# Optimization experiments

Hardware: AMD Instinct MI355X
Metric: run time of the kernel (lower is better)

## Reference

```python
import jax, jax.numpy as jnp
import numpy as np

NUM_GROUPS = 4
NUM_HEADS = 8
EPS = 1e-5


def setup_inputs() -> dict:
    key = jax.random.key(0)
    k1, k2, k3 = jax.random.split(key, 3)
    B, C, D, H, W = 4, 256, 32, 32, 32
    x = jax.random.normal(k1, (B, C, D, H, W), dtype=jnp.float32)
    gn_weight = jnp.ones((C,), dtype=jnp.float32)
    gn_bias = jnp.zeros((C,), dtype=jnp.float32)
    # 1x1x1 conv weights collapse to [out_ch, in_ch] matrices
    qkv_weight = jax.random.normal(k2, (3 * C, C), dtype=jnp.float32) * (1.0 / np.sqrt(C))
    out_weight = jax.random.normal(k3, (C, C), dtype=jnp.float32) * (1.0 / np.sqrt(C))
    out_bias = jnp.zeros((C,), dtype=jnp.float32)
    return {"x": x, "gn_weight": gn_weight, "gn_bias": gn_bias,
            "qkv_weight": qkv_weight, "out_weight": out_weight, "out_bias": out_bias}


def _group_norm(x, weight, bias):
    B, C, D, H, W = x.shape
    g = NUM_GROUPS
    xg = x.reshape(B, g, C // g, D, H, W)
    mean = jnp.mean(xg, axis=(2, 3, 4, 5), keepdims=True)
    var = jnp.var(xg, axis=(2, 3, 4, 5), keepdims=True)
    xn = ((xg - mean) * jax.lax.rsqrt(var + EPS)).reshape(B, C, D, H, W)
    return xn * weight[None, :, None, None, None] + bias[None, :, None, None, None]


def reference(x, gn_weight, gn_bias, qkv_weight, out_weight, out_bias):
    B, C, D, H, W = x.shape
    N = D * H * W
    hd = C // NUM_HEADS  # per-head channels

    norm = _group_norm(x, gn_weight, gn_bias)
    # 1x1x1 conv == channel matmul: [B,3C,D,H,W]
    qkv = jnp.einsum('bcdhw,oc->bodhw', norm, qkv_weight)
    # 'b (qkv heads c) d h w -> qkv b heads c (d h w)'
    qkv = qkv.reshape(B, 3, NUM_HEADS, hd, N)
    q, k, v = qkv[:, 0], qkv[:, 1], qkv[:, 2]  # each [B, heads, hd, N]

    k = jax.nn.softmax(k, axis=-1)  # softmax over spatial dim
    sim = jnp.einsum('bhdn,bhen->bhde', k, v)   # [B, heads, hd, hd]
    out = jnp.einsum('bhde,bhdn->bhen', sim, q)  # [B, heads, hd, N]
    out = out.reshape(B, C, D, H, W)

    out = jnp.einsum('bcdhw,oc->bodhw', out, out_weight) + out_bias[None, :, None, None, None]
    return out + x
```

## Files before the change

### kernel.cpp

```cpp
#include <hip/hip_runtime.h>
#include <cmath>


typedef __bf16 bf16x8 __attribute__((ext_vector_type(8)));
typedef float f32x4 __attribute__((ext_vector_type(4)));

union U16 { uint4 u; unsigned short s[8]; bf16x8 v; };

__device__ __forceinline__ float bf2f(unsigned short h) {
    unsigned int u = ((unsigned int)h) << 16;
    return __builtin_bit_cast(float, u);
}
__device__ __forceinline__ unsigned short f2bf(float f) {
    unsigned int u = __builtin_bit_cast(unsigned int, f);
    u = (u + 0x7fffu + ((u >> 16) & 1u)) >> 16;
    return (unsigned short)u;
}
__device__ __forceinline__ unsigned int pack2(unsigned short a, unsigned short b) {
    return (unsigned int)a | ((unsigned int)b << 16);
}

__global__ __launch_bounds__(64) void k_detect(const unsigned int* __restrict__ xr,
                                               int* __restrict__ flag) {
    unsigned int u = xr[threadIdx.x * 997];
    int e = (u >> 7) & 0xFF;
    bool ok = (e >= 100) && (e <= 141);
    unsigned long long m = __ballot(ok);
    if (threadIdx.x == 0) *flag = (__popcll(m) < 32) ? 1 : 0;
}

__global__ __launch_bounds__(256) void k_cvt_w(const void* __restrict__ qkvw,
                                               const void* __restrict__ outw,
                                               const void* __restrict__ gnw,
                                               const void* __restrict__ gnb,
                                               const void* __restrict__ outb,
                                               const int* __restrict__ flagp,
                                               unsigned short* __restrict__ wdst) {
    int idx = blockIdx.x * 256 + threadIdx.x;
    if (idx >= 262912) return;
    const void* src; int off;
    if      (idx < 196608) { src = qkvw; off = idx; }
    else if (idx < 262144) { src = outw; off = idx - 196608; }
    else if (idx < 262400) { src = gnw;  off = idx - 262144; }
    else if (idx < 262656) { src = gnb;  off = idx - 262400; }
    else                   { src = outb; off = idx - 262656; }
    int f = *flagp;
    wdst[idx] = f ? f2bf(((const float*)src)[off])
                  : ((const unsigned short*)src)[off];
}

__global__ __launch_bounds__(256) void k_cvt_x(const void* __restrict__ xr,
                                               const int* __restrict__ flagp,
                                               unsigned short* __restrict__ xw) {
    int f = *flagp;
    size_t base = ((size_t)blockIdx.x * 256 + threadIdx.x) * 8;
    if (f) {
        const float* xf = (const float*)xr;
        float4 a = *(const float4*)(xf + base);
        float4 c = *(const float4*)(xf + base + 4);
        U16 o;
        o.s[0] = f2bf(a.x); o.s[1] = f2bf(a.y); o.s[2] = f2bf(a.z); o.s[3] = f2bf(a.w);
        o.s[4] = f2bf(c.x); o.s[5] = f2bf(c.y); o.s[6] = f2bf(c.z); o.s[7] = f2bf(c.w);
        *(uint4*)(xw + base) = o.u;
    } else {
        *(uint4*)(xw + base) = *(const uint4*)((const unsigned short*)xr + base);
    }
}

__global__ __launch_bounds__(256) void k_gnsum(const unsigned short* __restrict__ x,
                                               float2* __restrict__ gn_part) {
    int t = threadIdx.x, bid = blockIdx.x;
    int grp = bid >> 7, chunk = bid & 127;
    const unsigned short* p = x + (size_t)grp * 2097152 + (size_t)chunk * 16384;
    float s = 0.f, q = 0.f;
    for (int i = 0; i < 8; i++) {
        U16 u; u.u = *(const uint4*)(p + i * 2048 + t * 8);
#pragma unroll
        for (int j = 0; j < 8; j++) { float f = bf2f(u.s[j]); s += f; q += f * f; }
    }
#pragma unroll
    for (int off = 32; off > 0; off >>= 1) { s += __shfl_xor(s, off); q += __shfl_xor(q, off); }
    __shared__ float rs[4], rq[4];
    int wave = t >> 6;
    if ((t & 63) == 0) { rs[wave] = s; rq[wave] = q; }
    __syncthreads();
    if (t == 0) gn_part[bid] = make_float2(rs[0] + rs[1] + rs[2] + rs[3],
                                           rq[0] + rq[1] + rq[2] + rq[3]);
}

__global__ __launch_bounds__(128) void k_gnfinal(const float2* __restrict__ gn_part,
                                                 float2* __restrict__ gstats) {
    int bg = blockIdx.x, t = threadIdx.x;
    float2 v = gn_part[bg * 128 + t];
    float s = v.x, q = v.y;
#pragma unroll
    for (int off = 32; off > 0; off >>= 1) { s += __shfl_xor(s, off); q += __shfl_xor(q, off); }
    __shared__ float rs[2], rq[2];
    if ((t & 63) == 0) { rs[t >> 6] = s; rq[t >> 6] = q; }
    __syncthreads();
    if (t == 0) {
        const float inv = 1.0f / 2097152.0f;
        float S = rs[0] + rs[1], Q = rq[0] + rq[1];
        float mean = S * inv;
        float var = Q * inv - mean * mean;
        gstats[bg] = make_float2(mean, rsqrtf(var + 1e-5f));
    }
}

__global__ __launch_bounds__(64) void k_beta(const unsigned short* __restrict__ wq,
                                             const unsigned short* __restrict__ wgnw,
                                             const unsigned short* __restrict__ wgnb,
                                             const float2* __restrict__ gstats,
                                             float* __restrict__ beta) {
    int bid = blockIdx.x;
    int b = bid / 768, o = bid % 768;
    int t = threadIdx.x, c = t * 4;
    float2 ms = gstats[b * 4 + (c >> 6)];
    uint2 qw = *(const uint2*)(wq + o * 256 + c);
    uint2 gw = *(const uint2*)(wgnw + c);
    uint2 gb = *(const uint2*)(wgnb + c);
    unsigned short qs[4] = {(unsigned short)(qw.x & 0xffff), (unsigned short)(qw.x >> 16),
                            (unsigned short)(qw.y & 0xffff), (unsigned short)(qw.y >> 16)};
    unsigned short wsx[4] = {(unsigned short)(gw.x & 0xffff), (unsigned short)(gw.x >> 16),
                             (unsigned short)(gw.y & 0xffff), (unsigned short)(gw.y >> 16)};
    unsigned short bs[4] = {(unsigned short)(gb.x & 0xffff), (unsigned short)(gb.x >> 16),
                            (unsigned short)(gb.y & 0xffff), (unsigned short)(gb.y >> 16)};
    float bacc = 0.f;
#pragma unroll
    for (int j = 0; j < 4; j++)
        bacc += bf2f(qs[j]) * (bf2f(bs[j]) - ms.x * ms.y * bf2f(wsx[j]));
#pragma unroll
    for (int off = 32; off > 0; off >>= 1) bacc += __shfl_xor(bacc, off);
    if (t == 0) beta[b * 768 + o] = bacc;
}

__global__ __launch_bounds__(256) void k_transpose(const unsigned short* __restrict__ x,
                                                   const unsigned short* __restrict__ wgnw,
                                                   const float2* __restrict__ gstats,
                                                   unsigned short* __restrict__ xt) {
    int tid = threadIdx.x, bid = blockIdx.x;
    int b = bid >> 11, r2 = bid & 2047, cblk = r2 >> 9, nblk = r2 & 511;
    float rstd = gstats[b * 4 + cblk].y;
    __shared__ __align__(16) unsigned short T[64 * 80];
    unsigned short tmp[2][8];
#pragma unroll
    for (int i = 0; i < 2; i++) {
        int crow = (tid >> 3) + 32 * i, nch = tid & 7;
        int c = cblk * 64 + crow;
        float sc = bf2f(wgnw[c]) * rstd;
        U16 u; u.u = *(const uint4*)(x + ((size_t)(b * 256 + c)) * 32768 + (size_t)nblk * 64 + nch * 8);
#pragma unroll
        for (int j = 0; j < 8; j++) tmp[i][j] = f2bf(bf2f(u.s[j]) * sc);
    }
#pragma unroll
    for (int i = 0; i < 2; i++) {
        int crow = (tid >> 3) + 32 * i, nch = tid & 7;
#pragma unroll
        for (int jj = 0; jj < 8; jj++) {
            int j = (jj + tid) & 7;
            T[(nch * 8 + j) * 80 + crow] = tmp[i][j];
        }
    }
    __syncthreads();
#pragma unroll
    for (int i = 0; i < 2; i++) {
        int nrow = (tid >> 3) + 32 * i, cch = tid & 7;
        uint4 v = *(const uint4*)&T[nrow * 80 + cch * 8];
        *(uint4*)(xt + ((size_t)b * 32768 + (size_t)nblk * 64 + nrow) * 256 + cblk * 64 + cch * 8) = v;
    }
}

__device__ __forceinline__ void stage128x64(const unsigned short* __restrict__ g,
                                            unsigned short* __restrict__ lds, int tid) {
    int wave = tid >> 6;
    int lane = tid & 63;
    int rsub = lane >> 3;
    int slot = lane & 7;
    uint4 v[4];
#pragma unroll
    for (int i = 0; i < 4; i++) {
        int row = wave * 32 + i * 8 + rsub;
        v[i] = *(const uint4*)(g + (size_t)row * 256 + slot * 8);
    }
#pragma unroll
    for (int i = 0; i < 4; i++) {
        int row = wave * 32 + i * 8 + rsub;
        int s = slot ^ (row & 7);
        *(uint4*)&lds[row * 64 + s * 8] = v[i];
    }
}

__device__ __forceinline__ void gemm_core(const unsigned short* __restrict__ A,
                                          const unsigned short* __restrict__ Bsrc,
                                          unsigned short* ldsA, unsigned short* ldsB,
                                          int tid, f32x4 (&acc)[4][4]) {
    int lane = tid & 63, l15 = lane & 15, quad = lane >> 4;
    int wave = tid >> 6, wm = wave & 1, wn = wave >> 1;
    for (int kt = 0; kt < 4; kt++) {
        stage128x64(A + kt * 64, ldsA, tid);
        stage128x64(Bsrc + kt * 64, ldsB, tid);
        __syncthreads();
#pragma unroll
        for (int ks = 0; ks < 2; ks++) {
            bf16x8 af[4], bv[4];
#pragma unroll
            for (int mi = 0; mi < 4; mi++) {
                int row = wm * 64 + mi * 16 + l15;
                af[mi] = *(const bf16x8*)&ldsA[row * 64 + (((ks * 4 + quad) ^ (row & 7)) * 8)];
            }
#pragma unroll
            for (int ni = 0; ni < 4; ni++) {
                int row = wn * 64 + ni * 16 + l15;
                bv[ni] = *(const bf16x8*)&ldsB[row * 64 + (((ks * 4 + quad) ^ (row & 7)) * 8)];
            }
#pragma unroll
            for (int mi = 0; mi < 4; mi++)
#pragma unroll
                for (int ni = 0; ni < 4; ni++)
                    acc[mi][ni] = __builtin_amdgcn_mfma_f32_16x16x32_bf16(af[mi], bv[ni], acc[mi][ni], 0, 0, 0);
        }
        __syncthreads();
    }
}

__global__ __launch_bounds__(256) void k_gemm1(const unsigned short* __restrict__ wq,
                                               const unsigned short* __restrict__ xt,
                                               const float* __restrict__ beta,
                                               unsigned short* __restrict__ qT,
                                               unsigned short* __restrict__ kv) {
    __shared__ __align__(16) unsigned short ldsbuf[2 * 128 * 64];
    unsigned short* ldsA = ldsbuf;
    unsigned short* ldsB = ldsbuf + 128 * 64;
    int tid = threadIdx.x, bid = blockIdx.x;
    int L = (bid & 7) * ((int)gridDim.x >> 3) + (bid >> 3);
    int mblk = L % 6;
    int t2 = L / 6;
    int nblk = t2 & 255, b = t2 >> 8;
    int o0 = mblk * 128;
    size_t n0 = (size_t)nblk * 128;
    const unsigned short* A = wq + (size_t)o0 * 256;
    const unsigned short* Bx = xt + ((size_t)b * 32768 + n0) * 256;
    f32x4 acc[4][4] = {};
    gemm_core(A, Bx, ldsA, ldsB, tid, acc);

    int lane = tid & 63, l15 = lane & 15, quad = lane >> 4;
    int wave = tid >> 6, wm = wave & 1, wn = wave >> 1;
    bool isQ = (mblk < 2);
    if (isQ) {
#pragma unroll
        for (int mi = 0; mi < 4; mi++) {
            int o_l = wm * 64 + mi * 16 + quad * 4;
            float4 be = *(const float4*)(beta + b * 768 + o0 + o_l);
#pragma unroll
            for (int ni = 0; ni < 4; ni++) {
                int n_l = wn * 64 + ni * 16 + l15;
                f32x4 v = acc[mi][ni];
                uint2 pv;
                pv.x = pack2(f2bf(v[0] + be.x), f2bf(v[1] + be.y));
                pv.y = pack2(f2bf(v[2] + be.z), f2bf(v[3] + be.w));
                *(uint2*)&ldsbuf[(n_l * 128 + o_l) ^ ((n_l & 7) << 3)] = pv;
            }
        }
        __syncthreads();
#pragma unroll
        for (int p = 0; p < 8; p++) {
            int n_l = p * 16 + (tid >> 4);
            int ch = tid & 15;
            uint4 v = *(const uint4*)&ldsbuf[(n_l * 128 + ch * 8) ^ ((n_l & 7) << 3)];
            *(uint4*)(qT + ((size_t)b * 32768 + n0 + n_l) * 256 + o0 + ch * 8) = v;
        }
    } else {
#pragma unroll
        for (int mi = 0; mi < 4; mi++) {
            int o_l = wm * 64 + mi * 16 + quad * 4;
            float4 be = *(const float4*)(beta + b * 768 + o0 + o_l);
            float bev[4] = {be.x, be.y, be.z, be.w};
#pragma unroll
            for (int ni = 0; ni < 4; ni++) {
                int n_l = wn * 64 + ni * 16 + l15;
                f32x4 v = acc[mi][ni];
#pragma unroll
                for (int r = 0; r < 4; r++) {
                    int o_r = o_l + r;
                    ldsbuf[(o_r * 128 + n_l) ^ ((o_r & 7) << 3)] = f2bf(v[r] + bev[r]);
                }
            }
        }
        __syncthreads();
        int kv0 = o0 - 256;
#pragma unroll
        for (int p = 0; p < 8; p++) {
            int o_r = p * 16 + (tid >> 4);
            int ch = tid & 15;
            uint4 v = *(const uint4*)&ldsbuf[(o_r * 128 + ch * 8) ^ ((o_r & 7) << 3)];
            *(uint4*)(kv + ((size_t)b * 512 + kv0 + o_r) * 32768 + n0 + ch * 8) = v;
        }
    }
}

__global__ __launch_bounds__(256) void k_stats(const unsigned short* __restrict__ kv,
                                               float2* __restrict__ stats) {
    int row = blockIdx.x, t = threadIdx.x;
    const unsigned short* p = kv + ((size_t)(row >> 8) * 512 + (row & 255)) * 32768;
    float m = -3.0e38f;
    for (int i = 0; i < 16; i++) {
        U16 u; u.u = *(const uint4*)(p + i * 2048 + t * 8);
#pragma unroll
        for (int j = 0; j < 8; j++) m = fmaxf(m, bf2f(u.s[j]));
    }
#pragma unroll
    for (int off = 32; off > 0; off >>= 1) m = fmaxf(m, __shfl_xor(m, off));
    __shared__ float rm[4], rs[4];
    int wave = t >> 6;
    if ((t & 63) == 0) rm[wave] = m;
    __syncthreads();
    m = fmaxf(fmaxf(rm[0], rm[1]), fmaxf(rm[2], rm[3]));
    float s = 0.f;
    for (int i = 0; i < 16; i++) {
        U16 u; u.u = *(const uint4*)(p + i * 2048 + t * 8);
#pragma unroll
        for (int j = 0; j < 8; j++) s += __expf(bf2f(u.s[j]) - m);
    }
#pragma unroll
    for (int off = 32; off > 0; off >>= 1) s += __shfl_xor(s, off);
    if ((t & 63) == 0) rs[wave] = s;
    __syncthreads();
    if (t == 0) stats[row] = make_float2(m, 1.0f / (rs[0] + rs[1] + rs[2] + rs[3]));
}

__global__ __launch_bounds__(64) void k_sim(const unsigned short* __restrict__ kv,
                                            const float2* __restrict__ stats,
                                            float* __restrict__ partials) {
    int bid = blockIdx.x;
    int bh = bid >> 6, chunk = bid & 63;
    int b = bh >> 3, h = bh & 7;
    int lane = threadIdx.x, l15 = lane & 15, quad = lane >> 4;
    size_t n0 = (size_t)chunk * 512 + quad * 8;
    float mrow[2], isr[2];
#pragma unroll
    for (int mi = 0; mi < 2; mi++) {
        float2 st = stats[b * 256 + h * 32 + mi * 16 + l15];
        mrow[mi] = st.x; isr[mi] = st.y;
    }
    const unsigned short* kb = kv + ((size_t)b * 512 + h * 32) * 32768;
    const unsigned short* vb = kv + ((size_t)b * 512 + 256 + h * 32) * 32768;
    f32x4 acc[2][2] = {};
    for (int t = 0; t < 16; t++) {
        size_t n = n0 + t * 32;
        bf16x8 af[2], bv[2];
#pragma unroll
        for (int mi = 0; mi < 2; mi++) {
            U16 u; u.u = *(const uint4*)(kb + (size_t)(mi * 16 + l15) * 32768 + n);
            U16 pv;
#pragma unroll
            for (int j = 0; j < 8; j++) pv.s[j] = f2bf(__expf(bf2f(u.s[j]) - mrow[mi]) * isr[mi]);
            af[mi] = pv.v;
        }
#pragma unroll
        for (int ni = 0; ni < 2; ni++) {
            U16 u; u.u = *(const uint4*)(vb + (size_t)(ni * 16 + l15) * 32768 + n);
            bv[ni] = u.v;
        }
#pragma unroll
        for (int mi = 0; mi < 2; mi++)
#pragma unroll
            for (int ni = 0; ni < 2; ni++)
                acc[mi][ni] = __builtin_amdgcn_mfma_f32_16x16x32_bf16(af[mi], bv[ni], acc[mi][ni], 0, 0, 0);
    }
    float* po = partials + (size_t)(bh * 64 + chunk) * 1024;
#pragma unroll
    for (int mi = 0; mi < 2; mi++)
#pragma unroll
        for (int ni = 0; ni < 2; ni++)
#pragma unroll
            for (int rr = 0; rr < 4; rr++)
                po[(mi * 16 + quad * 4 + rr) * 32 + ni * 16 + l15] = acc[mi][ni][rr];
}

__global__ __launch_bounds__(256) void k_combine(const float* __restrict__ partials,
                                                 float* __restrict__ sim) {
    int bh = blockIdx.x, tid = threadIdx.x;
#pragma unroll
    for (int i = 0; i < 4; i++) {
        float a = 0.f;
        const float* p = partials + (size_t)bh * 65536 + tid + i * 256;
        for (int c = 0; c < 64; c++) a += p[(size_t)c * 1024];
        sim[bh * 1024 + tid + i * 256] = a;
    }
}

__global__ __launch_bounds__(256) void k_buildM(const unsigned short* __restrict__ wo,
                                                const float* __restrict__ sim,
                                                unsigned short* __restrict__ M) {
    int bid = blockIdx.x, tid = threadIdx.x;
    int b = bid >> 8, o = bid & 255;
    __shared__ float lw[256];
    __shared__ float ls[8192];
    lw[tid] = bf2f(wo[o * 256 + tid]);
#pragma unroll
    for (int i = 0; i < 32; i++) ls[tid + i * 256] = sim[(size_t)b * 8192 + tid + i * 256];
    __syncthreads();
    int h = tid >> 5, d = tid & 31;
    float a = 0.f;
#pragma unroll
    for (int e = 0; e < 32; e++) {
        int ee = (e + d) & 31;
        a += lw[h * 32 + ee] * ls[h * 1024 + d * 32 + ee];
    }
    M[((size_t)b * 256 + o) * 256 + tid] = f2bf(a);
}

__global__ __launch_bounds__(256) void k_gemm2(const unsigned short* __restrict__ qT,
                                               const unsigned short* __restrict__ M,
                                               const unsigned short* __restrict__ wob,
                                               const void* __restrict__ xr,
                                               const int* __restrict__ flagp,
                                               void* __restrict__ outv,
                                               int b0) {
    __shared__ __align__(16) unsigned short ldsbuf[2 * 128 * 64];
    unsigned short* ldsA = ldsbuf;
    unsigned short* ldsB = ldsbuf + 128 * 64;
    float* ldsF = (float*)ldsbuf;
    int tid = threadIdx.x, bid = blockIdx.x;
    int L = (bid & 7) * ((int)gridDim.x >> 3) + (bid >> 3);
    int oblk = L & 1;
    int t2 = L >> 1;
    int mblk = t2 & 255, b = t2 >> 8;
    size_t n0 = (size_t)mblk * 128;
    int o0 = oblk * 128;
    const unsigned short* A = qT + ((size_t)b * 32768 + n0) * 256;
    const unsigned short* Bm = M + ((size_t)b * 256 + o0) * 256;
    f32x4 acc[4][4] = {};
    gemm_core(A, Bm, ldsA, ldsB, tid, acc);

    int f = *flagp;
    int gb = b0 + b;
    int lane = tid & 63, l15 = lane & 15, quad = lane >> 4;
    int wave = tid >> 6, wm = wave & 1, wn = wave >> 1;
    for (int half = 0; half < 2; half++) {
        if (wn == half) {
#pragma unroll
            for (int mi = 0; mi < 4; mi++) {
#pragma unroll
                for (int ni = 0; ni < 4; ni++) {
                    int o_h = ni * 16 + l15;
                    f32x4 v = acc[mi][ni];
#pragma unroll
                    for (int r = 0; r < 4; r++) {
                        int n_l = wm * 64 + mi * 16 + quad * 4 + r;
                        ldsF[(o_h * 128 + n_l) ^ ((o_h & 15) << 2)] = v[r];
                    }
                }
            }
        }
        __syncthreads();
#pragma unroll
        for (int p = 0; p < 8; p++) {
            int o_h = p * 8 + (tid >> 5);
            int ch = tid & 31;
            float4 v = *(const float4*)&ldsF[(o_h * 128 + ch * 4) ^ ((o_h & 15) << 2)];
            int o = o0 + half * 64 + o_h;
            float bias = bf2f(wob[o]);
            size_t base = ((size_t)gb * 256 + o) * 32768 + n0 + ch * 4;
            if (f) {
                float4 xv = *(const float4*)((const float*)xr + base);
                float4 ov = make_float4(v.x + bias + xv.x, v.y + bias + xv.y,
                                        v.z + bias + xv.z, v.w + bias + xv.w);
                *(float4*)((float*)outv + base) = ov;
            } else {
                uint2 xr2 = *(const uint2*)((const unsigned short*)xr + base);
                unsigned short xs[4] = {(unsigned short)(xr2.x & 0xffff), (unsigned short)(xr2.x >> 16),
                                        (unsigned short)(xr2.y & 0xffff), (unsigned short)(xr2.y >> 16)};
                uint2 pv;
                pv.x = pack2(f2bf(v.x + bias + bf2f(xs[0])), f2bf(v.y + bias + bf2f(xs[1])));
                pv.y = pack2(f2bf(v.z + bias + bf2f(xs[2])), f2bf(v.w + bias + bf2f(xs[3])));
                *(uint2*)((unsigned short*)outv + base) = pv;
            }
        }
        __syncthreads();
    }
}

extern "C" void kernel_launch(void* const* d_in, const int* in_sizes, int n_in,
                              void* d_out, int out_size, void* d_ws, size_t ws_size,
                              hipStream_t stream) {
    const void* x    = d_in[0];
    const void* gnw  = d_in[1];
    const void* gnb  = d_in[2];
    const void* qkvw = d_in[3];
    const void* outw = d_in[4];
    const void* outb = d_in[5];
    char* ws = (char*)d_ws;

    unsigned short* xw    = (unsigned short*)(ws);
    unsigned short* wdst  = (unsigned short*)(ws + 67108864);
    int*            flag  = (int*)(ws + 68157440);
    float2*         gstats= (float2*)(ws + 68157456);
    float*          beta  = (float*)(ws + 68158464);
    float2*         stats = (float2*)(ws + 68174848);
    const size_t passbase = 69206016;

    const unsigned short* wq   = wdst;
    const unsigned short* wo   = wdst + 196608;
    const unsigned short* wgnw = wdst + 262144;
    const unsigned short* wgnb = wdst + 262400;
    const unsigned short* wob  = wdst + 262656;

    int nb;
    if      (ws_size >= passbase + 4ull * 67108864) nb = 4;
    else if (ws_size >= passbase + 2ull * 67108864) nb = 2;
    else                                            nb = 1;

    size_t qT_off = passbase;
    size_t kv_off = passbase + (size_t)nb * 16777216;
    size_t xt_off = kv_off + (size_t)nb * 33554432;

    unsigned short* qT = (unsigned short*)(ws + qT_off);
    unsigned short* kv = (unsigned short*)(ws + kv_off);
    unsigned short* xt = (unsigned short*)(ws + xt_off);
    float2* gn_part    = (float2*)(ws + kv_off);
    unsigned short* M  = (unsigned short*)(ws + kv_off);
    float* partials    = (float*)(ws + xt_off);
    float* sim         = (float*)(ws + xt_off + (size_t)nb * 2097152);

    k_detect<<<dim3(1), dim3(64), 0, stream>>>((const unsigned int*)x, flag);
    k_cvt_w<<<dim3(1027), dim3(256), 0, stream>>>(qkvw, outw, gnw, gnb, outb, flag, wdst);
    k_cvt_x<<<dim3(16384), dim3(256), 0, stream>>>(x, flag, xw);

    for (int pass = 0; pass < 4; pass += nb) {
        const unsigned short* xp = xw + (size_t)pass * 8388608;
        k_gnsum    <<<dim3(512 * nb),  dim3(256), 0, stream>>>(xp, gn_part);
        k_gnfinal  <<<dim3(4 * nb),    dim3(128), 0, stream>>>(gn_part, gstats);
        k_beta     <<<dim3(768 * nb),  dim3(64),  0, stream>>>(wq, wgnw, wgnb, gstats, beta);
        k_transpose<<<dim3(2048 * nb), dim3(256), 0, stream>>>(xp, wgnw, gstats, xt);
        k_gemm1    <<<dim3(1536 * nb), dim3(256), 0, stream>>>(wq, xt, beta, qT, kv);
        k_stats    <<<dim3(256 * nb),  dim3(256), 0, stream>>>(kv, stats);
        k_sim      <<<dim3(512 * nb),  dim3(64),  0, stream>>>(kv, stats, partials);
        k_combine  <<<dim3(8 * nb),    dim3(256), 0, stream>>>(partials, sim);
        k_buildM   <<<dim3(256 * nb),  dim3(256), 0, stream>>>(wo, sim, M);
        k_gemm2    <<<dim3(512 * nb),  dim3(256), 0, stream>>>(qT, M, wob, x, flag, d_out, pass);
    }
}
```

Measured before the change: 591.5 us.

## Fold Q projection into output GEMM and drop bf16 copy of x

The Q projection is no longer materialized. Its weights are folded algebraically into the per-batch output matrix (G = M·Wq), stored as a split hi/lo bf16 pair, and the final GEMM runs directly on the normalized transposed x with K=512. The standalone fp32→bf16 conversion of x is removed, so GroupNorm stats and the transpose read the raw input directly and run once outside the pass loop. The GEMM core also gains register prefetch of the next K tile. In exchange there are extra small kernels (buildG, gamma), a doubled K in gemm2, and possible precision differences from the hi/lo split.

Result: slower. 801.0 us (+35.4%).

```diff
diff --git a/kernel.cpp b/kernel.cpp
--- a/kernel.cpp
+++ b/kernel.cpp
@@ -37,46 +37,47 @@
                                                const int* __restrict__ flagp,
                                                unsigned short* __restrict__ wdst) {
     int idx = blockIdx.x * 256 + threadIdx.x;
-    if (idx >= 262912) return;
+    if (idx >= 328448) return;
+    int f = *flagp;
     const void* src; int off;
     if      (idx < 196608) { src = qkvw; off = idx; }
     else if (idx < 262144) { src = outw; off = idx - 196608; }
     else if (idx < 262400) { src = gnw;  off = idx - 262144; }
     else if (idx < 262656) { src = gnb;  off = idx - 262400; }
-    else                   { src = outb; off = idx - 262656; }
-    int f = *flagp;
+    else if (idx < 262912) { src = outb; off = idx - 262656; }
+    else {
+        int i = idx - 262912;
+        int c = i >> 8, d = i & 255;
+        src = qkvw; off = d * 256 + c;
+    }
     wdst[idx] = f ? f2bf(((const float*)src)[off])
                   : ((const unsigned short*)src)[off];
 }
 
-__global__ __launch_bounds__(256) void k_cvt_x(const void* __restrict__ xr,
+__global__ __launch_bounds__(256) void k_gnsum(const void* __restrict__ xr,
                                                const int* __restrict__ flagp,
-                                               unsigned short* __restrict__ xw) {
-    int f = *flagp;
-    size_t base = ((size_t)blockIdx.x * 256 + threadIdx.x) * 8;
-    if (f) {
-        const float* xf = (const float*)xr;
-        float4 a = *(const float4*)(xf + base);
-        float4 c = *(const float4*)(xf + base + 4);
-        U16 o;
-        o.s[0] = f2bf(a.x); o.s[1] = f2bf(a.y); o.s[2] = f2bf(a.z); o.s[3] = f2bf(a.w);
-        o.s[4] = f2bf(c.x); o.s[5] = f2bf(c.y); o.s[6] = f2bf(c.z); o.s[7] = f2bf(c.w);
-        *(uint4*)(xw + base) = o.u;
-    } else {
-        *(uint4*)(xw + base) = *(const uint4*)((const unsigned short*)xr + base);
-    }
-}
-
-__global__ __launch_bounds__(256) void k_gnsum(const unsigned short* __restrict__ x,
                                                float2* __restrict__ gn_part) {
     int t = threadIdx.x, bid = blockIdx.x;
     int grp = bid >> 7, chunk = bid & 127;
-    const unsigned short* p = x + (size_t)grp * 2097152 + (size_t)chunk * 16384;
+    size_t base = (size_t)grp * 2097152 + (size_t)chunk * 16384;
+    int f = *flagp;
     float s = 0.f, q = 0.f;
-    for (int i = 0; i < 8; i++) {
-        U16 u; u.u = *(const uint4*)(p + i * 2048 + t * 8);
-#pragma unroll
-        for (int j = 0; j < 8; j++) { float f = bf2f(u.s[j]); s += f; q += f * f; }
+    if (f) {
+        const float* p = (const float*)xr + base;
+        for (int i = 0; i < 8; i++) {
+            float4 a = *(const float4*)(p + i * 2048 + t * 8);
+            float4 b = *(const float4*)(p + i * 2048 + t * 8 + 4);
+            float v[8] = {a.x, a.y, a.z, a.w, b.x, b.y, b.z, b.w};
+#pragma unroll
+            for (int j = 0; j < 8; j++) { s += v[j]; q += v[j] * v[j]; }
+        }
+    } else {
+        const unsigned short* p = (const unsigned short*)xr + base;
+        for (int i = 0; i < 8; i++) {
+            U16 u; u.u = *(const uint4*)(p + i * 2048 + t * 8);
+#pragma unroll
+            for (int j = 0; j < 8; j++) { float v = bf2f(u.s[j]); s += v; q += v * v; }
+        }
     }
 #pragma unroll
     for (int off = 32; off > 0; off >>= 1) { s += __shfl_xor(s, off); q += __shfl_xor(q, off); }
@@ -134,13 +135,15 @@
     if (t == 0) beta[b * 768 + o] = bacc;
 }
 
-__global__ __launch_bounds__(256) void k_transpose(const unsigned short* __restrict__ x,
-                                                   const unsigned short* __restrict__ wgnw,
-                                                   const float2* __restrict__ gstats,
-                                                   unsigned short* __restrict__ xt) {
+__global__ __launch_bounds__(256) void k_cvt_t(const void* __restrict__ xr,
+                                               const int* __restrict__ flagp,
+                                               const unsigned short* __restrict__ wgnw,
+                                               const float2* __restrict__ gstats,
+                                               unsigned short* __restrict__ xt) {
     int tid = threadIdx.x, bid = blockIdx.x;
     int b = bid >> 11, r2 = bid & 2047, cblk = r2 >> 9, nblk = r2 & 511;
     float rstd = gstats[b * 4 + cblk].y;
+    int f = *flagp;
     __shared__ __align__(16) unsigned short T[64 * 80];
     unsigned short tmp[2][8];
 #pragma unroll
@@ -148,9 +151,20 @@
         int crow = (tid >> 3) + 32 * i, nch = tid & 7;
         int c = cblk * 64 + crow;
         float sc = bf2f(wgnw[c]) * rstd;
-        U16 u; u.u = *(const uint4*)(x + ((size_t)(b * 256 + c)) * 32768 + (size_t)nblk * 64 + nch * 8);
-#pragma unroll
-        for (int j = 0; j < 8; j++) tmp[i][j] = f2bf(bf2f(u.s[j]) * sc);
+        size_t base = ((size_t)(b * 256 + c)) * 32768 + (size_t)nblk * 64 + nch * 8;
+        float v[8];
+        if (f) {
+            float4 a = *(const float4*)((const float*)xr + base);
+            float4 d = *(const float4*)((const float*)xr + base + 4);
+            v[0] = a.x; v[1] = a.y; v[2] = a.z; v[3] = a.w;
+            v[4] = d.x; v[5] = d.y; v[6] = d.z; v[7] = d.w;
+        } else {
+            U16 u; u.u = *(const uint4*)((const unsigned short*)xr + base);
+#pragma unroll
+            for (int j = 0; j < 8; j++) v[j] = bf2f(u.s[j]);
+        }
+#pragma unroll
+        for (int j = 0; j < 8; j++) tmp[i][j] = f2bf(v[j] * sc);
     }
 #pragma unroll
     for (int i = 0; i < 2; i++) {
@@ -170,55 +184,69 @@
     }
 }
 
-__device__ __forceinline__ void stage128x64(const unsigned short* __restrict__ g,
-                                            unsigned short* __restrict__ lds, int tid) {
-    int wave = tid >> 6;
-    int lane = tid & 63;
-    int rsub = lane >> 3;
-    int slot = lane & 7;
-    uint4 v[4];
+__device__ __forceinline__ void ld128x64(const unsigned short* __restrict__ g, int stride,
+                                         int tid, uint4 (&v)[4]) {
+    int wave = tid >> 6, lane = tid & 63;
+    const unsigned short* gl = g + (size_t)(lane >> 3) * stride + (lane & 7) * 8;
+#pragma unroll
+    for (int i = 0; i < 4; i++)
+        v[i] = *(const uint4*)(gl + (size_t)(wave * 32 + i * 8) * stride);
+}
+
+__device__ __forceinline__ void st128x64(unsigned short* __restrict__ lds, int tid,
+                                         const uint4 (&v)[4]) {
+    int wave = tid >> 6, lane = tid & 63;
 #pragma unroll
     for (int i = 0; i < 4; i++) {
-        int row = wave * 32 + i * 8 + rsub;
-        v[i] = *(const uint4*)(g + (size_t)row * 256 + slot * 8);
-    }
-#pragma unroll
-    for (int i = 0; i < 4; i++) {
-        int row = wave * 32 + i * 8 + rsub;
-        int s = slot ^ (row & 7);
+        int row = wave * 32 + i * 8 + (lane >> 3);
+        int s = (lane & 7) ^ (row & 7);
         *(uint4*)&lds[row * 64 + s * 8] = v[i];
     }
 }
 
+__device__ __forceinline__ void mfma_tile(const unsigned short* __restrict__ ldsA,
+                                          const unsigned short* __restrict__ ldsB,
+                                          int l15, int quad, int wm, int wn,
+                                          f32x4 (&acc)[4][4]) {
+#pragma unroll
+    for (int ks = 0; ks < 2; ks++) {
+        bf16x8 af[4], bv[4];
+#pragma unroll
+        for (int mi = 0; mi < 4; mi++) {
+            int row = wm * 64 + mi * 16 + l15;
+            af[mi] = *(const bf16x8*)&ldsA[row * 64 + (((ks * 4 + quad) ^ (row & 7)) * 8)];
+        }
+#pragma unroll
+        for (int ni = 0; ni < 4; ni++) {
+            int row = wn * 64 + ni * 16 + l15;
+            bv[ni] = *(const bf16x8*)&ldsB[row * 64 + (((ks * 4 + quad) ^ (row & 7)) * 8)];
+        }
+#pragma unroll
+        for (int mi = 0; mi < 4; mi++)
+#pragma unroll
+            for (int ni = 0; ni < 4; ni++)
+                acc[mi][ni] = __builtin_amdgcn_mfma_f32_16x16x32_bf16(af[mi], bv[ni], acc[mi][ni], 0, 0, 0);
+    }
+}
+
 __device__ __forceinline__ void gemm_core(const unsigned short* __restrict__ A,
-                                          const unsigned short* __restrict__ Bsrc,
+                                          const unsigned short* __restrict__ B,
                                           unsigned short* ldsA, unsigned short* ldsB,
                                           int tid, f32x4 (&acc)[4][4]) {
     int lane = tid & 63, l15 = lane & 15, quad = lane >> 4;
     int wave = tid >> 6, wm = wave & 1, wn = wave >> 1;
+    uint4 ra[4], rb[4];
+    ld128x64(A, 256, tid, ra);
+    ld128x64(B, 256, tid, rb);
     for (int kt = 0; kt < 4; kt++) {
-        stage128x64(A + kt * 64, ldsA, tid);
-        stage128x64(Bsrc + kt * 64, ldsB, tid);
+        st128x64(ldsA, tid, ra);
+        st128x64(ldsB, tid, rb);
         __syncthreads();
-#pragma unroll
-        for (int ks = 0; ks < 2; ks++) {
-            bf16x8 af[4], bv[4];
-#pragma unroll
-            for (int mi = 0; mi < 4; mi++) {
-                int row = wm * 64 + mi * 16 + l15;
-                af[mi] = *(const bf16x8*)&ldsA[row * 64 + (((ks * 4 + quad) ^ (row & 7)) * 8)];
-            }
-#pragma unroll
-            for (int ni = 0; ni < 4; ni++) {
-                int row = wn * 64 + ni * 16 + l15;
-                bv[ni] = *(const bf16x8*)&ldsB[row * 64 + (((ks * 4 + quad) ^ (row & 7)) * 8)];
-            }
-#pragma unroll
-            for (int mi = 0; mi < 4; mi++)
-#pragma unroll
-                for (int ni = 0; ni < 4; ni++)
-                    acc[mi][ni] = __builtin_amdgcn_mfma_f32_16x16x32_bf16(af[mi], bv[ni], acc[mi][ni], 0, 0, 0);
-        }
+        if (kt < 3) {
+            ld128x64(A + (kt + 1) * 64, 256, tid, ra);
+            ld128x64(B + (kt + 1) * 64, 256, tid, rb);
+        }
+        mfma_tile(ldsA, ldsB, l15, quad, wm, wn, acc);
         __syncthreads();
     }
 }
@@ -226,75 +254,50 @@
 __global__ __launch_bounds__(256) void k_gemm1(const unsigned short* __restrict__ wq,
                                                const unsigned short* __restrict__ xt,
                                                const float* __restrict__ beta,
-                                               unsigned short* __restrict__ qT,
-                                               unsigned short* __restrict__ kv) {
+                                               unsigned short* __restrict__ kv,
+                                               int b0) {
     __shared__ __align__(16) unsigned short ldsbuf[2 * 128 * 64];
     unsigned short* ldsA = ldsbuf;
     unsigned short* ldsB = ldsbuf + 128 * 64;
     int tid = threadIdx.x, bid = blockIdx.x;
     int L = (bid & 7) * ((int)gridDim.x >> 3) + (bid >> 3);
-    int mblk = L % 6;
-    int t2 = L / 6;
-    int nblk = t2 & 255, b = t2 >> 8;
-    int o0 = mblk * 128;
+    int mblk = L & 3;
+    int t2 = L >> 2;
+    int nblk = t2 & 255, bl = t2 >> 8;
+    int gb = b0 + bl;
+    int o0 = 256 + mblk * 128;
     size_t n0 = (size_t)nblk * 128;
     const unsigned short* A = wq + (size_t)o0 * 256;
-    const unsigned short* Bx = xt + ((size_t)b * 32768 + n0) * 256;
+    const unsigned short* B = xt + ((size_t)gb * 32768 + n0) * 256;
     f32x4 acc[4][4] = {};
-    gemm_core(A, Bx, ldsA, ldsB, tid, acc);
+    gemm_core(A, B, ldsA, ldsB, tid, acc);
 
     int lane = tid & 63, l15 = lane & 15, quad = lane >> 4;
     int wave = tid >> 6, wm = wave & 1, wn = wave >> 1;
-    bool isQ = (mblk < 2);
-    if (isQ) {
-#pragma unroll
-        for (int mi = 0; mi < 4; mi++) {
-            int o_l = wm * 64 + mi * 16 + quad * 4;
-            float4 be = *(const float4*)(beta + b * 768 + o0 + o_l);
-#pragma unroll
-            for (int ni = 0; ni < 4; ni++) {
-                int n_l = wn * 64 + ni * 16 + l15;
-                f32x4 v = acc[mi][ni];
-                uint2 pv;
-                pv.x = pack2(f2bf(v[0] + be.x), f2bf(v[1] + be.y));
-                pv.y = pack2(f2bf(v[2] + be.z), f2bf(v[3] + be.w));
-                *(uint2*)&ldsbuf[(n_l * 128 + o_l) ^ ((n_l & 7) << 3)] = pv;
+#pragma unroll
+    for (int mi = 0; mi < 4; mi++) {
+        int o_l = wm * 64 + mi * 16 + quad * 4;
+        float4 be = *(const float4*)(beta + gb * 768 + o0 + o_l);
+        float bev[4] = {be.x, be.y, be.z, be.w};
+#pragma unroll
+        for (int ni = 0; ni < 4; ni++) {
+            int n_l = wn * 64 + ni * 16 + l15;
+            f32x4 v = acc[mi][ni];
+#pragma unroll
+            for (int r = 0; r < 4; r++) {
+                int o_r = o_l + r;
+                ldsbuf[(o_r * 128 + n_l) ^ ((o_r & 7) << 3)] = f2bf(v[r] + bev[r]);
             }
         }
-        __syncthreads();
-#pragma unroll
-        for (int p = 0; p < 8; p++) {
-            int n_l = p * 16 + (tid >> 4);
-            int ch = tid & 15;
-            uint4 v = *(const uint4*)&ldsbuf[(n_l * 128 + ch * 8) ^ ((n_l & 7) << 3)];
-            *(uint4*)(qT + ((size_t)b * 32768 + n0 + n_l) * 256 + o0 + ch * 8) = v;
-        }
-    } else {
-#pragma unroll
-        for (int mi = 0; mi < 4; mi++) {
-            int o_l = wm * 64 + mi * 16 + quad * 4;
-            float4 be = *(const float4*)(beta + b * 768 + o0 + o_l);
-            float bev[4] = {be.x, be.y, be.z, be.w};
-#pragma unroll
-            for (int ni = 0; ni < 4; ni++) {
-                int n_l = wn * 64 + ni * 16 + l15;
-                f32x4 v = acc[mi][ni];
-#pragma unroll
-                for (int r = 0; r < 4; r++) {
-                    int o_r = o_l + r;
-                    ldsbuf[(o_r * 128 + n_l) ^ ((o_r & 7) << 3)] = f2bf(v[r] + bev[r]);
-                }
-            }
-        }
-        __syncthreads();
-        int kv0 = o0 - 256;
-#pragma unroll
-        for (int p = 0; p < 8; p++) {
-            int o_r = p * 16 + (tid >> 4);
-            int ch = tid & 15;
-            uint4 v = *(const uint4*)&ldsbuf[(o_r * 128 + ch * 8) ^ ((o_r & 7) << 3)];
-            *(uint4*)(kv + ((size_t)b * 512 + kv0 + o_r) * 32768 + n0 + ch * 8) = v;
-        }
+    }
+    __syncthreads();
+    int kv0 = mblk * 128;
+#pragma unroll
+    for (int p = 0; p < 8; p++) {
+        int o_r = p * 16 + (tid >> 4);
+        int ch = tid & 15;
+        uint4 v = *(const uint4*)&ldsbuf[(o_r * 128 + ch * 8) ^ ((o_r & 7) << 3)];
+        *(uint4*)(kv + ((size_t)bl * 512 + kv0 + o_r) * 32768 + n0 + ch * 8) = v;
     }
 }
 
@@ -378,22 +381,22 @@
 }
 
 __global__ __launch_bounds__(256) void k_combine(const float* __restrict__ partials,
-                                                 float* __restrict__ sim) {
+                                                 float* __restrict__ sim, int b0) {
     int bh = blockIdx.x, tid = threadIdx.x;
 #pragma unroll
     for (int i = 0; i < 4; i++) {
         float a = 0.f;
         const float* p = partials + (size_t)bh * 65536 + tid + i * 256;
         for (int c = 0; c < 64; c++) a += p[(size_t)c * 1024];
-        sim[bh * 1024 + tid + i * 256] = a;
+        sim[(size_t)(b0 * 8 + bh) * 1024 + tid + i * 256] = a;
     }
 }
 
 __global__ __launch_bounds__(256) void k_buildM(const unsigned short* __restrict__ wo,
                                                 const float* __restrict__ sim,
-                                                unsigned short* __restrict__ M) {
+                                                unsigned short* __restrict__ M, int b0) {
     int bid = blockIdx.x, tid = threadIdx.x;
-    int b = bid >> 8, o = bid & 255;
+    int b = b0 + (bid >> 8), o = bid & 255;
     __shared__ float lw[256];
     __shared__ float ls[8192];
     lw[tid] = bf2f(wo[o * 256 + tid]);
@@ -410,9 +413,63 @@
     M[((size_t)b * 256 + o) * 256 + tid] = f2bf(a);
 }
 
-__global__ __launch_bounds__(256) void k_gemm2(const unsigned short* __restrict__ qT,
-                                               const unsigned short* __restrict__ M,
-                                               const unsigned short* __restrict__ wob,
+__global__ __launch_bounds__(256) void k_buildG(const unsigned short* __restrict__ M,
+                                                const unsigned short* __restrict__ wqT,
+                                                unsigned short* __restrict__ G2, int b0) {
+    __shared__ __align__(16) unsigned short ldsbuf[2 * 128 * 64];
+    unsigned short* ldsA = ldsbuf;
+    unsigned short* ldsB = ldsbuf + 128 * 64;
+    int tid = threadIdx.x, bid = blockIdx.x;
+    int b = b0 + (bid >> 2), t = bid & 3;
+    int o0 = (t >> 1) * 128, c0 = (t & 1) * 128;
+    const unsigned short* A = M + (size_t)b * 65536 + (size_t)o0 * 256;
+    const unsigned short* B = wqT + (size_t)c0 * 256;
+    f32x4 acc[4][4] = {};
+    gemm_core(A, B, ldsA, ldsB, tid, acc);
+
+    int lane = tid & 63, l15 = lane & 15, quad = lane >> 4;
+    int wave = tid >> 6, wm = wave & 1, wn = wave >> 1;
+#pragma unroll
+    for (int mi = 0; mi < 4; mi++) {
+        int o_l = o0 + wm * 64 + mi * 16 + quad * 4;
+#pragma unroll
+        for (int ni = 0; ni < 4; ni++) {
+            int c_l = c0 + wn * 64 + ni * 16 + l15;
+            f32x4 v = acc[mi][ni];
+#pragma unroll
+            for (int r = 0; r < 4; r++) {
+                float g = v[r];
+                unsigned short hi = f2bf(g);
+                unsigned short lo = f2bf(g - bf2f(hi));
+                size_t rb = (size_t)b * 131072 + (size_t)(o_l + r) * 512 + c_l;
+                G2[rb] = hi;
+                G2[rb + 256] = lo;
+            }
+        }
+    }
+}
+
+__global__ __launch_bounds__(64) void k_gamma(const unsigned short* __restrict__ M,
+                                              const float* __restrict__ beta,
+                                              const unsigned short* __restrict__ wob,
+                                              float* __restrict__ gamma, int b0) {
+    int bid = blockIdx.x;
+    int b = b0 + (bid >> 8), o = bid & 255;
+    int t = threadIdx.x, c = t * 4;
+    uint2 mw = *(const uint2*)(M + (size_t)b * 65536 + o * 256 + c);
+    float4 bq = *(const float4*)(beta + b * 768 + c);
+    float acc = bf2f((unsigned short)(mw.x & 0xffff)) * bq.x
+              + bf2f((unsigned short)(mw.x >> 16))    * bq.y
+              + bf2f((unsigned short)(mw.y & 0xffff)) * bq.z
+              + bf2f((unsigned short)(mw.y >> 16))    * bq.w;
+#pragma unroll
+    for (int off = 32; off > 0; off >>= 1) acc += __shfl_xor(acc, off);
+    if (t == 0) gamma[b * 256 + o] = acc + bf2f(wob[o]);
+}
+
+__global__ __launch_bounds__(256) void k_gemm2(const unsigned short* __restrict__ xt,
+                                               const unsigned short* __restrict__ G2,
+                                               const float* __restrict__ gamma,
                                                const void* __restrict__ xr,
                                                const int* __restrict__ flagp,
                                                void* __restrict__ outv,
@@ -425,18 +482,32 @@
     int L = (bid & 7) * ((int)gridDim.x >> 3) + (bid >> 3);
     int oblk = L & 1;
     int t2 = L >> 1;
-    int mblk = t2 & 255, b = t2 >> 8;
+    int mblk = t2 & 255, bl = t2 >> 8;
+    int gb = b0 + bl;
     size_t n0 = (size_t)mblk * 128;
     int o0 = oblk * 128;
-    const unsigned short* A = qT + ((size_t)b * 32768 + n0) * 256;
-    const unsigned short* Bm = M + ((size_t)b * 256 + o0) * 256;
-    f32x4 acc[4][4] = {};
-    gemm_core(A, Bm, ldsA, ldsB, tid, acc);
-
-    int f = *flagp;
-    int gb = b0 + b;
+    const unsigned short* A = xt + ((size_t)gb * 32768 + n0) * 256;
+    const unsigned short* Bg = G2 + (size_t)gb * 131072 + (size_t)o0 * 512;
+
     int lane = tid & 63, l15 = lane & 15, quad = lane >> 4;
     int wave = tid >> 6, wm = wave & 1, wn = wave >> 1;
+    f32x4 acc[4][4] = {};
+    uint4 ra[4], rb[4];
+    ld128x64(A, 256, tid, ra);
+    ld128x64(Bg, 512, tid, rb);
+    for (int kt = 0; kt < 8; kt++) {
+        st128x64(ldsA, tid, ra);
+        st128x64(ldsB, tid, rb);
+        __syncthreads();
+        if (kt < 7) {
+            ld128x64(A + ((kt + 1) & 3) * 64, 256, tid, ra);
+            ld128x64(Bg + (kt + 1) * 64, 512, tid, rb);
+        }
+        mfma_tile(ldsA, ldsB, l15, quad, wm, wn, acc);
+        __syncthreads();
+    }
+
+    int f = *flagp;
     for (int half = 0; half < 2; half++) {
         if (wn == half) {
 #pragma unroll
@@ -460,7 +531,7 @@
             int ch = tid & 31;
             float4 v = *(const float4*)&ldsF[(o_h * 128 + ch * 4) ^ ((o_h & 15) << 2)];
             int o = o0 + half * 64 + o_h;
-            float bias = bf2f(wob[o]);
+            float bias = gamma[gb * 256 + o];
             size_t base = ((size_t)gb * 256 + o) * 32768 + n0 + ch * 4;
             if (f) {
                 float4 xv = *(const float4*)((const float*)xr + base);
@@ -492,52 +563,49 @@
     const void* outb = d_in[5];
     char* ws = (char*)d_ws;
 
-    unsigned short* xw    = (unsigned short*)(ws);
-    unsigned short* wdst  = (unsigned short*)(ws + 67108864);
-    int*            flag  = (int*)(ws + 68157440);
-    float2*         gstats= (float2*)(ws + 68157456);
-    float*          beta  = (float*)(ws + 68158464);
-    float2*         stats = (float2*)(ws + 68174848);
-    const size_t passbase = 69206016;
+    unsigned short* xt   = (unsigned short*)(ws);
+    unsigned short* wdst = (unsigned short*)(ws + 67108864);
+    char* sm = ws + 68157440;
+    int*    flag    = (int*)(sm);
+    float2* gstats  = (float2*)(sm + 64);
+    float*  beta    = (float*)(sm + 1024);
+    float2* stats   = (float2*)(sm + 16384);
+    float*  gamma   = (float*)(sm + 24576);
+    float2* gn_part = (float2*)(sm + 32768);
+    float*  sim     = (float*)(sm + 65536);
+    unsigned short* M  = (unsigned short*)(sm + 262144);
+    unsigned short* G2 = (unsigned short*)(sm + 786432);
+    const size_t kv_off = 70254592;
 
     const unsigned short* wq   = wdst;
     const unsigned short* wo   = wdst + 196608;
     const unsigned short* wgnw = wdst + 262144;
     const unsigned short* wgnb = wdst + 262400;
     const unsigned short* wob  = wdst + 262656;
-
-    int nb;
-    if      (ws_size >= passbase + 4ull * 67108864) nb = 4;
-    else if (ws_size >= passbase + 2ull * 67108864) nb = 2;
-    else                                            nb = 1;
-
-    size_t qT_off = passbase;
-    size_t kv_off = passbase + (size_t)nb * 16777216;
-    size_t xt_off = kv_off + (size_t)nb * 33554432;
-
-    unsigned short* qT = (unsigned short*)(ws + qT_off);
+    const unsigned short* wqT  = wdst + 262912;
+
+    int nb = 1;
+    if      (ws_size >= kv_off + 4ull * (33554432 + 2097152)) nb = 4;
+    else if (ws_size >= kv_off + 2ull * (33554432 + 2097152)) nb = 2;
+
     unsigned short* kv = (unsigned short*)(ws + kv_off);
-    unsigned short* xt = (unsigned short*)(ws + xt_off);
-    float2* gn_part    = (float2*)(ws + kv_off);
-    unsigned short* M  = (unsigned short*)(ws + kv_off);
-    float* partials    = (float*)(ws + xt_off);
-    float* sim         = (float*)(ws + xt_off + (size_t)nb * 2097152);
-
-    k_detect<<<dim3(1), dim3(64), 0, stream>>>((const unsigned int*)x, flag);
-    k_cvt_w<<<dim3(1027), dim3(256), 0, stream>>>(qkvw, outw, gnw, gnb, outb, flag, wdst);
-    k_cvt_x<<<dim3(16384), dim3(256), 0, stream>>>(x, flag, xw);
+    float* partials    = (float*)(ws + kv_off + (size_t)nb * 33554432);
+
+    k_detect <<<dim3(1),    dim3(64),  0, stream>>>((const unsigned int*)x, flag);
+    k_cvt_w  <<<dim3(1283), dim3(256), 0, stream>>>(qkvw, outw, gnw, gnb, outb, flag, wdst);
+    k_gnsum  <<<dim3(2048), dim3(256), 0, stream>>>(x, flag, gn_part);
+    k_gnfinal<<<dim3(16),   dim3(128), 0, stream>>>(gn_part, gstats);
+    k_beta   <<<dim3(3072), dim3(64),  0, stream>>>(wq, wgnw, wgnb, gstats, beta);
+    k_cvt_t  <<<dim3(8192), dim3(256), 0, stream>>>(x, flag, wgnw, gstats, xt);
 
     for (int pass = 0; pass < 4; pass += nb) {
-        const unsigned short* xp = xw + (size_t)pass * 8388608;
-        k_gnsum    <<<dim3(512 * nb),  dim3(256), 0, stream>>>(xp, gn_part);
-        k_gnfinal  <<<dim3(4 * nb),    dim3(128), 0, stream>>>(gn_part, gstats);
-        k_beta     <<<dim3(768 * nb),  dim3(64),  0, stream>>>(wq, wgnw, wgnb, gstats, beta);
-        k_transpose<<<dim3(2048 * nb), dim3(256), 0, stream>>>(xp, wgnw, gstats, xt);
-        k_gemm1    <<<dim3(1536 * nb), dim3(256), 0, stream>>>(wq, xt, beta, qT, kv);
-        k_stats    <<<dim3(256 * nb),  dim3(256), 0, stream>>>(kv, stats);
-        k_sim      <<<dim3(512 * nb),  dim3(64),  0, stream>>>(kv, stats, partials);
-        k_combine  <<<dim3(8 * nb),    dim3(256), 0, stream>>>(partials, sim);
-        k_buildM   <<<dim3(256 * nb),  dim3(256), 0, stream>>>(wo, sim, M);
-        k_gemm2    <<<dim3(512 * nb),  dim3(256), 0, stream>>>(qT, M, wob, x, flag, d_out, pass);
-    }
-}
+        k_gemm1  <<<dim3(1024 * nb), dim3(256), 0, stream>>>(wq, xt, beta, kv, pass);
+        k_stats  <<<dim3(256 * nb),  dim3(256), 0, stream>>>(kv, stats);
+        k_sim    <<<dim3(512 * nb),  dim3(64),  0, stream>>>(kv, stats, partials);
+        k_combine<<<dim3(8 * nb),    dim3(256), 0, stream>>>(partials, sim, pass);
+        k_buildM <<<dim3(256 * nb),  dim3(256), 0, stream>>>(wo, sim, M, pass);
+        k_buildG <<<dim3(4 * nb),    dim3(256), 0, stream>>>(M, wqT, G2, pass);
+        k_gamma  <<<dim3(256 * nb),  dim3(64),  0, stream>>>(M, beta, wob, gamma, pass);
+        k_gemm2  <<<dim3(512 * nb),  dim3(256), 0, stream>>>(xt, G2, gamma, x, flag, d_out, pass);
+    }
+}
```
